# Kernel optimization log

Measured on AMD Instinct MI355X. Metric: run time of the kernel, lower is better.

## Reference

```python
import jax, jax.numpy as jnp
import numpy as np

B, L, D, O = 4, 256, 512, 128

def setup_inputs() -> dict:
    key = jax.random.key(0)
    k1, k2, k3, k4, k5, k6 = jax.random.split(key, 6)
    return {
        "x1": jax.random.normal(k1, (B, L, D), jnp.float32),
        "x2": jax.random.normal(k2, (B, L, D), jnp.float32),
        "bw": jax.random.uniform(k3, (2,), jnp.float32),
        "W_bil": jax.random.normal(k4, (O, D + 1, D + 1), jnp.float32) * 0.02,
        "W_lin": jax.random.normal(k5, (2 * D, O), jnp.float32) * 0.02,
        "b_lin": jax.random.normal(k6, (O,), jnp.float32) * 0.02,
    }

def reference(x1, x2, bw, W_bil, W_lin, b_lin):
    bwn = jax.nn.softmax(bw)
    d1 = x1.shape[-1]
    # Bilinear with bias_x/bias_y: append ones column to x1 and x2.
    ones1 = jnp.ones((*x1.shape[:2], 1), x1.dtype)
    ones2 = jnp.ones((*x2.shape[:2], 1), x2.dtype)
    x1b = jnp.concatenate([x1, ones1], axis=-1)  # [B, L1, D+1]
    x2b = jnp.concatenate([x2, ones2], axis=-1)  # [B, L2, D+1]
    # einsum 'bxi,oij,byj->boxy' then permute(0,2,3,1) -> bxyo
    bilinear_logits = jnp.einsum('bxi,oij,byj->bxyo', x1b, W_bil, x2b)
    # linear over concat([x1 expanded, x2 expanded]) == split-weight broadcast sum
    lin1 = x1 @ W_lin[:d1]   # [B, L1, O]
    lin2 = x2 @ W_lin[d1:]   # [B, L2, O]
    linear_logits = lin1[:, :, None, :] + lin2[:, None, :, :] + b_lin  # [B, L1, L2, O]
    return bwn[0] * bilinear_logits + bwn[1] * linear_logits
```

## Files before the change

### kernel.cpp

```cpp
#include <hip/hip_runtime.h>


#define LL 256
#define DD 512
#define OO 128
#define BB 4
#define WB_OI 263169
#define WB_R512 262656

typedef __attribute__((ext_vector_type(8))) short  short8;
typedef __attribute__((ext_vector_type(8))) unsigned short us8;
typedef __attribute__((ext_vector_type(4))) unsigned short us4;
typedef __attribute__((ext_vector_type(4))) float  f32x4;

__device__ __forceinline__ unsigned short f2bf(float f) {
    unsigned int u = __builtin_bit_cast(unsigned int, f);
    u = (u + 0x7FFFu + ((u >> 16) & 1u)) >> 16;
    return (unsigned short)u;
}
__device__ __forceinline__ float bf2f(unsigned short s) {
    return __builtin_bit_cast(float, (unsigned int)s << 16);
}
__device__ __forceinline__ void load_lds16(const void* g, void* l) {
    __builtin_amdgcn_global_load_lds(
        (const __attribute__((address_space(1))) unsigned int*)g,
        (__attribute__((address_space(3))) unsigned int*)l, 16, 0, 0);
}

__global__ __launch_bounds__(256) void castprep_kernel(
    const float* __restrict__ x1, const float* __restrict__ x2,
    unsigned short* __restrict__ x1b, unsigned short* __restrict__ x2b,
    const float* __restrict__ Wb, float* __restrict__ W512T)
{
    const int bid = blockIdx.x;
    if (bid < 1024) {
        int i = bid * 256 + threadIdx.x;
        const float* s; unsigned short* d; int j;
        if (i < 131072) { s = x1; d = x1b; j = i; }
        else            { s = x2; d = x2b; j = i - 131072; }
        float4 v = ((const float4*)s)[j];
        us4 u; u.x = f2bf(v.x); u.y = f2bf(v.y); u.z = f2bf(v.z); u.w = f2bf(v.w);
        *(us4*)(d + (size_t)j * 4) = u;
    } else {
        int idx = (bid - 1024) * 256 + threadIdx.x;
        if (idx < 513 * 128) {
            const int o = idx & 127, j = idx >> 7;
            W512T[idx] = Wb[(size_t)o * WB_OI + WB_R512 + j];
        }
    }
}

__global__ __launch_bounds__(256) void prepw_kernel(
    const float* __restrict__ Wb, const float* __restrict__ bw,
    unsigned short* __restrict__ Wb16)
{
    const int t = threadIdx.x;
    const int row = blockIdx.x * 4 + (t >> 6);
    const int o = row >> 9, i = row & 511;
    const int l = t & 63;
    const float e0 = __expf(bw[0]), e1 = __expf(bw[1]);
    const float bwn0 = e0 / (e0 + e1);
    const float* src = Wb + (size_t)o * WB_OI + (size_t)i * 513;
    unsigned short* dst = Wb16 + (size_t)row * 512;
    float v[8];
    #pragma unroll
    for (int e = 0; e < 8; ++e) v[e] = src[e * 64 + l];
    #pragma unroll
    for (int e = 0; e < 8; ++e) dst[e * 64 + l] = f2bf(bwn0 * v[e]);
}

__global__ __launch_bounds__(128) void u512_kernel(
    const float* __restrict__ x2, const float* __restrict__ W512T,
    const float* __restrict__ W_lin, const float* __restrict__ b_lin,
    const float* __restrict__ bw, float* __restrict__ u512buf)
{
    __shared__ float xs[DD];
    const int by = blockIdx.x;
    const int o  = threadIdx.x;
    const float* xr = x2 + (size_t)by * DD;
    for (int j = o; j < DD; j += 128) xs[j] = xr[j];
    __syncthreads();
    float s1 = W512T[512 * 128 + o];
    float s2 = b_lin[o];
    #pragma unroll 4
    for (int j = 0; j < DD; ++j) {
        s1 += xs[j] * W512T[j * 128 + o];
        s2 += xs[j] * W_lin[(size_t)(DD + j) * OO + o];
    }
    const float e0 = __expf(bw[0]), e1 = __expf(bw[1]);
    const float bwn0 = e0 / (e0 + e1), bwn1 = e1 / (e0 + e1);
    u512buf[(size_t)by * OO + o] = bwn0 * s1 + bwn1 * s2;
}

__global__ __launch_bounds__(256, 4) void passA_kernel(
    const unsigned short* __restrict__ x2b, const unsigned short* __restrict__ Wb16,
    const float* __restrict__ W_bil, const float* __restrict__ W_lin,
    const float* __restrict__ bw, unsigned short* __restrict__ Up)
{
    __shared__ __align__(16) char smem[33280];
    unsigned short* As0 = (unsigned short*)smem;
    unsigned short* Bs0 = (unsigned short*)(smem + 8192);
    unsigned short* As1 = (unsigned short*)(smem + 16384);
    unsigned short* Bs1 = (unsigned short*)(smem + 24576);
    unsigned short* Cs  = (unsigned short*)smem;
    float* corr = (float*)(smem + 32768);

    const int t = threadIdx.x, w = t >> 6, l = t & 63;
    const int ib = blockIdx.x * 128;
    const int yg = blockIdx.y * 128;
    const int o  = blockIdx.z;
    const int wy = w & 1, wx = w >> 1;

    f32x4 acc[4][4] = {};
    const unsigned short* Wo16 = Wb16 + (size_t)o * DD * DD;

    const int rb0 = w * 32;
    const int rr  = l >> 2;
    const int kof = ((l & 3) ^ ((l >> 3) & 3)) * 8;

#define STAGE_A(ASP, BSP, K0) do {                                              \
    _Pragma("unroll")                                                           \
    for (int q = 0; q < 2; ++q) {                                               \
        const int rb = rb0 + q * 16, rrow = rb + rr, ko = (K0) + kof;           \
        load_lds16(x2b  + (size_t)(yg + rrow) * DD + ko, (ASP) + rb * 32);      \
        load_lds16(Wo16 + (size_t)(ib + rrow) * DD + ko, (BSP) + rb * 32);      \
    } } while (0)

    STAGE_A(As0, Bs0, 0);
    __syncthreads();

    const int mrow = wy * 64 + (l & 15);
    const int ncol = wx * 64 + (l & 15);
    const int psel = ((l >> 4) ^ ((l >> 1) & 3)) * 8;

    #pragma unroll 2
    for (int kt = 0; kt < 16; ++kt) {
        const int cur = kt & 1;
        unsigned short* Asr = cur ? As1 : As0;
        unsigned short* Bsr = cur ? Bs1 : Bs0;
        unsigned short* Asn = cur ? As0 : As1;
        unsigned short* Bsn = cur ? Bs0 : Bs1;
        if (kt < 15) STAGE_A(Asn, Bsn, (kt + 1) * 32);
        short8 af[4], bfr[4];
        #pragma unroll
        for (int mt = 0; mt < 4; ++mt) af[mt]  = *(const short8*)(Asr + (mrow + mt * 16) * 32 + psel);
        #pragma unroll
        for (int nt = 0; nt < 4; ++nt) bfr[nt] = *(const short8*)(Bsr + (ncol + nt * 16) * 32 + psel);
        #pragma unroll
        for (int mt = 0; mt < 4; ++mt)
            #pragma unroll
            for (int nt = 0; nt < 4; ++nt)
                acc[mt][nt] = __builtin_amdgcn_mfma_f32_16x16x32_bf16(af[mt], bfr[nt], acc[mt][nt], 0, 0, 0);
        __syncthreads();
    }
#undef STAGE_A

    const float e0 = __expf(bw[0]), e1 = __expf(bw[1]);
    const float bwn0 = e0 / (e0 + e1), bwn1 = e1 / (e0 + e1);
    if (t < 128) {
        const int ig = ib + t;
        corr[t] = bwn1 * W_lin[(size_t)ig * OO + o]
                + bwn0 * W_bil[(size_t)o * WB_OI + (size_t)ig * 513 + 512];
    }
    #pragma unroll
    for (int half = 0; half < 2; ++half) {
        if (wy == half) {
            #pragma unroll
            for (int mt = 0; mt < 4; ++mt) {
                const int yl = mt * 16 + ((l >> 4) << 2);
                #pragma unroll
                for (int nt = 0; nt < 4; ++nt) {
                    const int ic = wx * 64 + nt * 16 + (l & 15);
                    #pragma unroll
                    for (int r = 0; r < 4; ++r)
                        Cs[(yl + r) * 136 + ic] = f2bf(acc[mt][nt][r]);
                }
            }
        }
        __syncthreads();
        #pragma unroll
        for (int p = 0; p < 4; ++p) {
            const int yl = p * 16 + (t >> 4);
            const int i0 = (t & 15) * 8;
            short8 v = *(const short8*)(Cs + yl * 136 + i0);
            us8 uo;
            #pragma unroll
            for (int e = 0; e < 8; ++e)
                uo[e] = f2bf(bf2f((unsigned short)v[e]) + corr[i0 + e]);
            *(us8*)(Up + ((size_t)(yg + half * 64 + yl) * OO + o) * DD + ib + i0) = uo;
        }
        __syncthreads();
    }
}

__global__ __launch_bounds__(256, 4) void passB_kernel(
    const unsigned short* __restrict__ x1b, const unsigned short* __restrict__ Up,
    const float* __restrict__ u512buf, float* __restrict__ out)
{
    __shared__ __align__(16) char smem[33280];
    unsigned short* As0 = (unsigned short*)smem;
    unsigned short* Bs0 = (unsigned short*)(smem + 8192);
    unsigned short* As1 = (unsigned short*)(smem + 16384);
    unsigned short* Bs1 = (unsigned short*)(smem + 24576);
    float* u5 = (float*)(smem + 32768);

    const int t = threadIdx.x, w = t >> 6, l = t & 63;
    const int xb = blockIdx.x * 128;
    const int yg = blockIdx.y;
    const int bb = yg >> 8, y = yg & 255;
    const int wy = w & 1, wx = w >> 1;
    if (t < 128) u5[t] = u512buf[(size_t)yg * OO + t];

    f32x4 acc[4][4] = {};

    const int rb0 = w * 32;
    const int rr  = l >> 2;
    const int kof = ((l & 3) ^ ((l >> 3) & 3)) * 8;

#define STAGE_B(ASP, BSP, K0) do {                                                   \
    _Pragma("unroll")                                                                \
    for (int q = 0; q < 2; ++q) {                                                    \
        const int rb = rb0 + q * 16, rrow = rb + rr, ko = (K0) + kof;                \
        load_lds16(x1b + (size_t)(bb * LL + xb + rrow) * DD + ko, (ASP) + rb * 32);  \
        load_lds16(Up  + (size_t)(yg * OO + rrow) * DD + ko,      (BSP) + rb * 32);  \
    } } while (0)

    STAGE_B(As0, Bs0, 0);
    __syncthreads();

    const int mrow = wy * 64 + (l & 15);
    const int ncol = wx * 64 + (l & 15);
    const int psel = ((l >> 4) ^ ((l >> 1) & 3)) * 8;

    #pragma unroll 2
    for (int kt = 0; kt < 16; ++kt) {
        const int cur = kt & 1;
        unsigned short* Asr = cur ? As1 : As0;
        unsigned short* Bsr = cur ? Bs1 : Bs0;
        unsigned short* Asn = cur ? As0 : As1;
        unsigned short* Bsn = cur ? Bs0 : Bs1;
        if (kt < 15) STAGE_B(Asn, Bsn, (kt + 1) * 32);
        short8 af[4], bfr[4];
        #pragma unroll
        for (int mt = 0; mt < 4; ++mt) af[mt]  = *(const short8*)(Asr + (mrow + mt * 16) * 32 + psel);
        #pragma unroll
        for (int nt = 0; nt < 4; ++nt) bfr[nt] = *(const short8*)(Bsr + (ncol + nt * 16) * 32 + psel);
        #pragma unroll
        for (int mt = 0; mt < 4; ++mt)
            #pragma unroll
            for (int nt = 0; nt < 4; ++nt)
                acc[mt][nt] = __builtin_amdgcn_mfma_f32_16x16x32_bf16(af[mt], bfr[nt], acc[mt][nt], 0, 0, 0);
        __syncthreads();
    }
#undef STAGE_B

    #pragma unroll
    for (int mt = 0; mt < 4; ++mt) {
        const int xr = wy * 64 + mt * 16 + ((l >> 4) << 2);
        #pragma unroll
        for (int nt = 0; nt < 4; ++nt) {
            const int oc = wx * 64 + nt * 16 + (l & 15);
            const float c = u5[oc];
            #pragma unroll
            for (int r = 0; r < 4; ++r)
                out[((size_t)(bb * LL + xb + xr + r) * LL + y) * OO + oc] = acc[mt][nt][r] + c;
        }
    }
}

extern "C" void kernel_launch(void* const* d_in, const int* in_sizes, int n_in,
                              void* d_out, int out_size, void* d_ws, size_t ws_size,
                              hipStream_t stream)
{
    const float* x1    = (const float*)d_in[0];
    const float* x2    = (const float*)d_in[1];
    const float* bw    = (const float*)d_in[2];
    const float* W_bil = (const float*)d_in[3];
    const float* W_lin = (const float*)d_in[4];
    const float* b_lin = (const float*)d_in[5];
    float* out = (float*)d_out;

    char* ws = (char*)d_ws;
    unsigned short* x1b16 = (unsigned short*)ws;
    unsigned short* x2b16 = (unsigned short*)(ws + (1u << 20));
    float*          u512b = (float*)(ws + (2u << 20));
    float*          W512T = (float*)(ws + (2u << 20) + (512u << 10));
    unsigned short* Wb16  = (unsigned short*)(ws + (3u << 20));
    unsigned short* Up    = (unsigned short*)(ws + (3u << 20) + ((size_t)128 * 512 * 512 * 2));

    castprep_kernel<<<1281, 256, 0, stream>>>(x1, x2, x1b16, x2b16, W_bil, W512T);
    prepw_kernel<<<16384, 256, 0, stream>>>(W_bil, bw, Wb16);
    u512_kernel<<<BB * LL, 128, 0, stream>>>(x2, W512T, W_lin, b_lin, bw, u512b);

    passA_kernel<<<dim3(4, 8, OO), 256, 0, stream>>>(x2b16, Wb16, W_bil, W_lin, bw, Up);
    passB_kernel<<<dim3(2, BB * LL), 256, 0, stream>>>(x1b16, Up, u512b, out);
}
```

Measured before the change: 452.3 us.

## Merge passB x-tiles into one 512-thread block and remap passA block order

passB now handles all 256 x rows for a given (b,y) in a single 512-thread block with 8 waves. Each Up tile is therefore loaded from global memory once instead of twice, and the x1b tile is shared across the block, at the cost of more LDS (about 48KB) and fewer blocks. passA switches to a 1D grid whose remapping interleaves block IDs (id&7 strided by 512), so that concurrently scheduled blocks spread across output channels and tiles. This is probably aimed at XCD/L2 locality on the chiplet GPU.

Result: no change. 457.6 us (+1.2%).

```diff
diff --git a/kernel.cpp b/kernel.cpp
--- a/kernel.cpp
+++ b/kernel.cpp
@@ -106,9 +106,11 @@
     float* corr = (float*)(smem + 32768);
 
     const int t = threadIdx.x, w = t >> 6, l = t & 63;
-    const int ib = blockIdx.x * 128;
-    const int yg = blockIdx.y * 128;
-    const int o  = blockIdx.z;
+    const int id  = blockIdx.x;
+    const int lin = (id & 7) * 512 + (id >> 3);
+    const int o   = lin >> 5;
+    const int ib  = (lin & 3) * 128;
+    const int yg  = ((lin >> 2) & 7) * 128;
     const int wy = w & 1, wx = w >> 1;
 
     f32x4 acc[4][4] = {};
@@ -193,58 +195,53 @@
     }
 }
 
-__global__ __launch_bounds__(256, 4) void passB_kernel(
+__global__ __launch_bounds__(512, 4) void passB_kernel(
     const unsigned short* __restrict__ x1b, const unsigned short* __restrict__ Up,
     const float* __restrict__ u512buf, float* __restrict__ out)
 {
-    __shared__ __align__(16) char smem[33280];
-    unsigned short* As0 = (unsigned short*)smem;
-    unsigned short* Bs0 = (unsigned short*)(smem + 8192);
-    unsigned short* As1 = (unsigned short*)(smem + 16384);
-    unsigned short* Bs1 = (unsigned short*)(smem + 24576);
-    float* u5 = (float*)(smem + 32768);
+    __shared__ __align__(16) char smem[49664];
+    float* u5 = (float*)(smem + 49152);
 
     const int t = threadIdx.x, w = t >> 6, l = t & 63;
-    const int xb = blockIdx.x * 128;
-    const int yg = blockIdx.y;
+    const int yg = blockIdx.x;
     const int bb = yg >> 8, y = yg & 255;
-    const int wy = w & 1, wx = w >> 1;
+    const int wxm = w >> 1, wxo = w & 1;
     if (t < 128) u5[t] = u512buf[(size_t)yg * OO + t];
 
     f32x4 acc[4][4] = {};
-
-    const int rb0 = w * 32;
-    const int rr  = l >> 2;
-    const int kof = ((l & 3) ^ ((l >> 3) & 3)) * 8;
-
-#define STAGE_B(ASP, BSP, K0) do {                                                   \
-    _Pragma("unroll")                                                                \
-    for (int q = 0; q < 2; ++q) {                                                    \
-        const int rb = rb0 + q * 16, rrow = rb + rr, ko = (K0) + kof;                \
-        load_lds16(x1b + (size_t)(bb * LL + xb + rrow) * DD + ko, (ASP) + rb * 32);  \
-        load_lds16(Up  + (size_t)(yg * OO + rrow) * DD + ko,      (BSP) + rb * 32);  \
-    } } while (0)
-
-    STAGE_B(As0, Bs0, 0);
+    const unsigned short* Abase = x1b + (size_t)bb * LL * DD;
+    const unsigned short* Bbase = Up + (size_t)yg * OO * DD;
+
+    const int arow = t >> 2;
+    const int kof  = ((t & 3) ^ ((t >> 3) & 3)) * 8;
+
+#define STAGE_B(S, K0) do {                                                     \
+    unsigned short* As_ = (unsigned short*)(smem + (S) * 24576);                \
+    unsigned short* Bs_ = As_ + 8192;                                           \
+    const int ko = (K0) + kof;                                                  \
+    load_lds16(Abase + (size_t)arow * DD + ko,         As_ + t * 8);            \
+    load_lds16(Abase + (size_t)(128 + arow) * DD + ko, As_ + 4096 + t * 8);     \
+    load_lds16(Bbase + (size_t)arow * DD + ko,         Bs_ + t * 8);            \
+  } while (0)
+
+    STAGE_B(0, 0);
     __syncthreads();
 
-    const int mrow = wy * 64 + (l & 15);
-    const int ncol = wx * 64 + (l & 15);
+    const int mrow = wxm * 64 + (l & 15);
+    const int ncol = wxo * 64 + (l & 15);
     const int psel = ((l >> 4) ^ ((l >> 1) & 3)) * 8;
 
     #pragma unroll 2
     for (int kt = 0; kt < 16; ++kt) {
         const int cur = kt & 1;
-        unsigned short* Asr = cur ? As1 : As0;
-        unsigned short* Bsr = cur ? Bs1 : Bs0;
-        unsigned short* Asn = cur ? As0 : As1;
-        unsigned short* Bsn = cur ? Bs0 : Bs1;
-        if (kt < 15) STAGE_B(Asn, Bsn, (kt + 1) * 32);
+        if (kt < 15) STAGE_B(cur ^ 1, (kt + 1) * 32);
+        const unsigned short* As_ = (const unsigned short*)(smem + cur * 24576);
+        const unsigned short* Bs_ = As_ + 8192;
         short8 af[4], bfr[4];
         #pragma unroll
-        for (int mt = 0; mt < 4; ++mt) af[mt]  = *(const short8*)(Asr + (mrow + mt * 16) * 32 + psel);
-        #pragma unroll
-        for (int nt = 0; nt < 4; ++nt) bfr[nt] = *(const short8*)(Bsr + (ncol + nt * 16) * 32 + psel);
+        for (int mt = 0; mt < 4; ++mt) af[mt]  = *(const short8*)(As_ + (mrow + mt * 16) * 32 + psel);
+        #pragma unroll
+        for (int nt = 0; nt < 4; ++nt) bfr[nt] = *(const short8*)(Bs_ + (ncol + nt * 16) * 32 + psel);
         #pragma unroll
         for (int mt = 0; mt < 4; ++mt)
             #pragma unroll
@@ -256,14 +253,14 @@
 
     #pragma unroll
     for (int mt = 0; mt < 4; ++mt) {
-        const int xr = wy * 64 + mt * 16 + ((l >> 4) << 2);
+        const int xr = wxm * 64 + mt * 16 + ((l >> 4) << 2);
         #pragma unroll
         for (int nt = 0; nt < 4; ++nt) {
-            const int oc = wx * 64 + nt * 16 + (l & 15);
+            const int oc = wxo * 64 + nt * 16 + (l & 15);
             const float c = u5[oc];
             #pragma unroll
             for (int r = 0; r < 4; ++r)
-                out[((size_t)(bb * LL + xb + xr + r) * LL + y) * OO + oc] = acc[mt][nt][r] + c;
+                out[((size_t)(bb * LL + xr + r) * LL + y) * OO + oc] = acc[mt][nt][r] + c;
         }
     }
 }
@@ -292,6 +289,6 @@
     prepw_kernel<<<16384, 256, 0, stream>>>(W_bil, bw, Wb16);
     u512_kernel<<<BB * LL, 128, 0, stream>>>(x2, W512T, W_lin, b_lin, bw, u512b);
 
-    passA_kernel<<<dim3(4, 8, OO), 256, 0, stream>>>(x2b16, Wb16, W_bil, W_lin, bw, Up);
-    passB_kernel<<<dim3(2, BB * LL), 256, 0, stream>>>(x1b16, Up, u512b, out);
-}
+    passA_kernel<<<4096, 256, 0, stream>>>(x2b16, Wb16, W_bil, W_lin, bw, Up);
+    passB_kernel<<<1024, 512, 0, stream>>>(x1b16, Up, u512b, out);
+}
```
